# Performance work log

Hardware: AMD Instinct MI355X
Metric: run time of the kernel (lower is better)

## Reference

```python
import jax, jax.numpy as jnp
import numpy as np

N_NODES = 100000
N_EDGES = 1200000
N_GRAPHS = 1024
IN_DIM, HIDDEN, OUT_DIM = 4, 64, 2
BN_EPS = 1e-5


def setup_inputs() -> dict:
    key = jax.random.key(0)
    ks = jax.random.split(key, 12)
    x = jax.random.normal(ks[0], (N_NODES, IN_DIM), dtype=jnp.float32)
    edge_index = jax.random.randint(ks[1], (2, N_EDGES), 0, N_NODES, dtype=jnp.int64)
    batch = jnp.sort(jax.random.randint(ks[2], (N_NODES,), 0, N_GRAPHS, dtype=jnp.int64))
    s = 1.0 / np.sqrt(HIDDEN)
    return {
        "x": x,
        "edge_index": edge_index,
        "batch": batch,
        "W_enc": jax.random.normal(ks[3], (IN_DIM, HIDDEN), dtype=jnp.float32) * 0.5,
        "b_enc": jnp.zeros((HIDDEN,), dtype=jnp.float32),
        "bn_gamma": jnp.ones((HIDDEN,), dtype=jnp.float32),
        "bn_beta": jnp.zeros((HIDDEN,), dtype=jnp.float32),
        "bn_mean": jax.random.normal(ks[4], (HIDDEN,), dtype=jnp.float32) * 0.1,
        "bn_var": jax.random.uniform(ks[5], (HIDDEN,), dtype=jnp.float32, minval=0.5, maxval=1.5),
        "W_gcn": jax.random.normal(ks[6], (HIDDEN, HIDDEN), dtype=jnp.float32) * s,
        "b_gcn": jnp.zeros((HIDDEN,), dtype=jnp.float32),
        "W_cls1": jax.random.normal(ks[7], (HIDDEN, HIDDEN), dtype=jnp.float32) * s,
        "b_cls1": jnp.zeros((HIDDEN,), dtype=jnp.float32),
        "W_cls2": jax.random.normal(ks[8], (HIDDEN, OUT_DIM), dtype=jnp.float32) * s,
        "b_cls2": jnp.zeros((OUT_DIM,), dtype=jnp.float32),
    }


def reference(x, edge_index, batch, W_enc, b_enc, bn_gamma, bn_beta, bn_mean, bn_var,
              W_gcn, b_gcn, W_cls1, b_cls1, W_cls2, b_cls2):
    n = x.shape[0]
    # Encoder: Linear -> ReLU -> Dropout(eval=identity) -> BatchNorm1d (running stats)
    h = jnp.maximum(x @ W_enc + b_enc, 0.0)
    h = (h - bn_mean) * jax.lax.rsqrt(bn_var + BN_EPS) * bn_gamma + bn_beta
    # GCNConv (PyG): add self-loops, symmetric deg^{-1/2} normalization
    loop = jnp.arange(n, dtype=edge_index.dtype)
    src = jnp.concatenate([edge_index[0], loop])  # [E+N]
    dst = jnp.concatenate([edge_index[1], loop])
    deg = jnp.zeros((n,), dtype=h.dtype).at[dst].add(1.0)
    dis = jnp.where(deg > 0, jax.lax.rsqrt(jnp.maximum(deg, 1.0)), 0.0)
    norm = dis[src] * dis[dst]  # [E+N]
    hw = h @ W_gcn  # [N, H]
    msg = hw[src] * norm[:, None]  # gather + scale, [E+N, H]
    agg = jax.ops.segment_sum(msg, dst, num_segments=n) + b_gcn
    agg = jnp.maximum(agg, 0.0)  # .relu()
    # global_mean_pool over graphs
    sums = jax.ops.segment_sum(agg, batch, num_segments=N_GRAPHS)  # [G, H]
    cnts = jax.ops.segment_sum(jnp.ones((n,), dtype=agg.dtype), batch, num_segments=N_GRAPHS)
    gm = sums / jnp.maximum(cnts, 1.0)[:, None]
    # Classifier: Linear -> ReLU -> Dropout(eval) -> Linear
    out = jnp.maximum(gm @ W_cls1 + b_cls1, 0.0) @ W_cls2 + b_cls2
    return out
```

## Files before the change

### kernel.cpp

```cpp
#include <hip/hip_runtime.h>

#define N_NODES  100000
#define N_EDGES  1200000
#define N_GRAPHS 1024

#define BSH    9
#define BNODES 512
#define NBUCK  196
#define FBLK   512
#define CHUNK  ((N_EDGES + FBLK - 1) / FBLK)
#define ENC_BLOCKS 1563

__device__ __forceinline__ unsigned short f2bf(float f) {
  unsigned u = __float_as_uint(f);
  return (unsigned short)((u + 0x7fffu + ((u >> 16) & 1u)) >> 16);
}
__device__ __forceinline__ float bf2f(unsigned short b) {
  return __uint_as_float(((unsigned)b) << 16);
}

__global__ __launch_bounds__(256) void k_cnt(const int* __restrict__ ei,
                                             int* __restrict__ cnt,
                                             float* __restrict__ gsum) {
  __shared__ int h[NBUCK];
  int t = threadIdx.x;
  for (int i = t; i < NBUCK; i += 256) h[i] = 0;
  int gi = blockIdx.x * 256 + t;
  if (gi < N_GRAPHS * 64) gsum[gi] = 0.f;
  __syncthreads();
  int start = blockIdx.x * CHUNK, end = min(start + CHUNK, N_EDGES);
  for (int e = start + t; e < end; e += 256)
    atomicAdd(&h[ei[N_EDGES + e] >> BSH], 1);
  __syncthreads();
  for (int b = t; b < NBUCK; b += 256)
    cnt[b * FBLK + blockIdx.x] = h[b];
}

__global__ __launch_bounds__(256) void k_scan_enc(
    int* __restrict__ cnt, int* __restrict__ tot,
    const float* __restrict__ x,
    const float* __restrict__ Wenc, const float* __restrict__ benc,
    const float* __restrict__ gamma, const float* __restrict__ beta,
    const float* __restrict__ mean,  const float* __restrict__ var,
    const float* __restrict__ Wgcn,
    unsigned short* __restrict__ hw) {
  int t = threadIdx.x;
  int lane = t & 63, w = t >> 6;
  if (blockIdx.x < NBUCK) {
    __shared__ int wsum[4];
    int b = blockIdx.x;
    int v0 = cnt[b * FBLK + 2 * t], v1 = cnt[b * FBLK + 2 * t + 1];
    int a = v0 + v1;
    int incl = a;
    #pragma unroll
    for (int off = 1; off < 64; off <<= 1) {
      int y = __shfl_up(incl, off);
      if (lane >= off) incl += y;
    }
    if (lane == 63) wsum[w] = incl;
    __syncthreads();
    if (t == 0) {
      int s = 0;
      #pragma unroll
      for (int i = 0; i < 4; ++i) { int x2 = wsum[i]; wsum[i] = s; s += x2; }
      tot[b] = s;
    }
    __syncthreads();
    int excl = wsum[w] + incl - a;
    cnt[b * FBLK + 2 * t] = excl;
    cnt[b * FBLK + 2 * t + 1] = excl + v0;
    return;
  }
  int wv = (blockIdx.x - NBUCK) * 4 + w;
  if (wv >= 6250) return;
  float be = benc[lane];
  float sc = gamma[lane] * rsqrtf(var[lane] + 1e-5f);
  float mu = mean[lane], bt = beta[lane];
  float w0 = Wenc[lane], w1 = Wenc[64 + lane], w2 = Wenc[128 + lane], w3 = Wenc[192 + lane];
  float wreg[64];
  #pragma unroll
  for (int k = 0; k < 64; ++k) wreg[k] = Wgcn[k * 64 + lane];
  int n0 = wv * 16;
  for (int i = 0; i < 16; ++i) {
    int n = n0 + i;
    float4 xv = ((const float4*)x)[n];
    float h = fmaf(xv.w, w3, fmaf(xv.z, w2, fmaf(xv.y, w1, fmaf(xv.x, w0, be))));
    h = fmaxf(h, 0.f);
    float hbn = (h - mu) * sc + bt;
    int hb = __float_as_int(hbn);
    float a0 = 0.f, a1 = 0.f, a2 = 0.f, a3 = 0.f;
    #pragma unroll
    for (int k = 0; k < 64; k += 4) {
      a0 = fmaf(__int_as_float(__builtin_amdgcn_readlane(hb, k)),     wreg[k],     a0);
      a1 = fmaf(__int_as_float(__builtin_amdgcn_readlane(hb, k + 1)), wreg[k + 1], a1);
      a2 = fmaf(__int_as_float(__builtin_amdgcn_readlane(hb, k + 2)), wreg[k + 2], a2);
      a3 = fmaf(__int_as_float(__builtin_amdgcn_readlane(hb, k + 3)), wreg[k + 3], a3);
    }
    hw[(size_t)n * 64 + lane] = f2bf((a0 + a1) + (a2 + a3));
  }
}

__global__ __launch_bounds__(256) void k_fill(const int* __restrict__ ei,
                                              const int* __restrict__ cnt,
                                              const int* __restrict__ tot,
                                              int* __restrict__ binned) {
  __shared__ int cur[NBUCK];
  __shared__ int wsum[4];
  int t = threadIdx.x, blk = blockIdx.x;
  int lane = t & 63, w = t >> 6;
  int v = (t < NBUCK) ? tot[t] : 0;
  int incl = v;
  #pragma unroll
  for (int off = 1; off < 64; off <<= 1) {
    int y = __shfl_up(incl, off);
    if (lane >= off) incl += y;
  }
  if (lane == 63) wsum[w] = incl;
  __syncthreads();
  if (t == 0) {
    int s = 0;
    #pragma unroll
    for (int i = 0; i < 4; ++i) { int x2 = wsum[i]; wsum[i] = s; s += x2; }
  }
  __syncthreads();
  if (t < NBUCK) cur[t] = (wsum[w] + incl - v) + cnt[t * FBLK + blk];
  __syncthreads();
  int start = blk * CHUNK, end = min(start + CHUNK, N_EDGES);
  for (int e = start + t; e < end; e += 256) {
    int src = ei[e];
    int dst = ei[N_EDGES + e];
    int b = dst >> BSH;
    int p = atomicAdd(&cur[b], 1);
    binned[p] = src | ((dst & (BNODES - 1)) << 17);
  }
}

__global__ __launch_bounds__(512) void k_csr(const int* __restrict__ tot,
                                             const int* __restrict__ binned,
                                             int* __restrict__ csr,
                                             int* __restrict__ row_start,
                                             float* __restrict__ dis) {
  __shared__ int hist[BNODES];
  __shared__ int wsum[8];
  __shared__ int b0S;
  int t = threadIdx.x;
  int blk = blockIdx.x;
  int lane = t & 63, w = t >> 6;
  int pv = (t < blk) ? tot[t] : 0;
  #pragma unroll
  for (int off = 32; off > 0; off >>= 1) pv += __shfl_down(pv, off);
  if (lane == 0) wsum[w] = pv;
  hist[t] = 0;
  __syncthreads();
  if (t == 0) {
    int s = 0;
    #pragma unroll
    for (int i = 0; i < 8; ++i) s += wsum[i];
    b0S = s;
  }
  __syncthreads();
  int b0 = b0S;
  int nE = tot[blk];
  int node0 = blk << BSH;
  for (int i = t; i < nE; i += 512)
    atomicAdd(&hist[(unsigned)binned[b0 + i] >> 17], 1);
  __syncthreads();
  int v = hist[t];
  int incl = v;
  #pragma unroll
  for (int off = 1; off < 64; off <<= 1) {
    int y = __shfl_up(incl, off);
    if (lane >= off) incl += y;
  }
  if (lane == 63) wsum[w] = incl;
  __syncthreads();
  if (t == 0) {
    int s = 0;
    #pragma unroll
    for (int i = 0; i < 8; ++i) { int x2 = wsum[i]; wsum[i] = s; s += x2; }
  }
  __syncthreads();
  int excl = wsum[w] + incl - v;
  hist[t] = excl;
  int node = node0 + t;
  if (node < N_NODES) {
    row_start[node] = b0 + excl;
    dis[node] = rsqrtf((float)(v + 1));
  }
  if (t == 0 && blk == NBUCK - 1) row_start[N_NODES] = N_EDGES;
  __syncthreads();
  for (int i = t; i < nE; i += 512) {
    int vv = binned[b0 + i];
    int d = (unsigned)vv >> 17;
    int p = atomicAdd(&hist[d], 1);
    csr[b0 + p] = vv & 0x1FFFF;
  }
}

__global__ __launch_bounds__(64) void k_gather(
    const int* __restrict__ row_start, const int* __restrict__ csr,
    const float* __restrict__ dis, const unsigned short* __restrict__ hw,
    const int* __restrict__ batch, const float* __restrict__ bgcn,
    float* __restrict__ gsum) {
  int lane = threadIdx.x;
  int nb = blockIdx.x * 4;
  float bias = bgcn[lane];
  float vout[4];
  int gid[4];
  #pragma unroll
  for (int k = 0; k < 4; ++k) {
    int n = nb + k;
    int st = row_start[n], en = row_start[n + 1];
    float dn = rsqrtf((float)(en - st + 1));
    float a0 = 0.f, a1 = 0.f, a2 = 0.f, a3 = 0.f;
    for (int c = st; c < en; c += 64) {
      int m = min(64, en - c);
      int idx = c + lane;
      int chunk = 0; float dv = 0.f;
      if (idx < en) { chunk = csr[idx]; dv = dis[chunk]; }
      int dvb = __float_as_int(dv);
      int j = 0;
      for (; j + 4 <= m; j += 4) {
        int s0 = __builtin_amdgcn_readlane(chunk, j);
        int s1 = __builtin_amdgcn_readlane(chunk, j + 1);
        int s2 = __builtin_amdgcn_readlane(chunk, j + 2);
        int s3 = __builtin_amdgcn_readlane(chunk, j + 3);
        float d0 = __int_as_float(__builtin_amdgcn_readlane(dvb, j));
        float d1 = __int_as_float(__builtin_amdgcn_readlane(dvb, j + 1));
        float d2 = __int_as_float(__builtin_amdgcn_readlane(dvb, j + 2));
        float d3 = __int_as_float(__builtin_amdgcn_readlane(dvb, j + 3));
        a0 = fmaf(d0, bf2f(hw[(size_t)s0 * 64 + lane]), a0);
        a1 = fmaf(d1, bf2f(hw[(size_t)s1 * 64 + lane]), a1);
        a2 = fmaf(d2, bf2f(hw[(size_t)s2 * 64 + lane]), a2);
        a3 = fmaf(d3, bf2f(hw[(size_t)s3 * 64 + lane]), a3);
      }
      for (; j < m; ++j) {
        int s = __builtin_amdgcn_readlane(chunk, j);
        float d = __int_as_float(__builtin_amdgcn_readlane(dvb, j));
        a0 = fmaf(d, bf2f(hw[(size_t)s * 64 + lane]), a0);
      }
    }
    float self = bf2f(hw[(size_t)n * 64 + lane]);
    float sum = (a0 + a1) + (a2 + a3);
    vout[k] = fmaxf(dn * fmaf(dn, self, sum) + bias, 0.f);
    gid[k] = batch[n];
  }
  float vs = vout[0];
  int cg = gid[0];
  #pragma unroll
  for (int k = 1; k < 4; ++k) {
    if (gid[k] == cg) vs += vout[k];
    else {
      atomicAdd(&gsum[cg * 64 + lane], vs);
      vs = vout[k]; cg = gid[k];
    }
  }
  atomicAdd(&gsum[cg * 64 + lane], vs);
}

__global__ void k_cls(const float* __restrict__ gsum, const int* __restrict__ batch,
                      const float* __restrict__ W1, const float* __restrict__ b1,
                      const float* __restrict__ W2, const float* __restrict__ b2,
                      float* __restrict__ out) {
  __shared__ float gm[64];
  __shared__ int cntS;
  int j = threadIdx.x;
  int g = blockIdx.x;
  if (j == 0) {
    int lo = 0, hi = N_NODES;
    while (lo < hi) { int mid = (lo + hi) >> 1; if (batch[mid] < g) lo = mid + 1; else hi = mid; }
    int lo2 = lo, hi2 = N_NODES;
    while (lo2 < hi2) { int mid = (lo2 + hi2) >> 1; if (batch[mid] < g + 1) lo2 = mid + 1; else hi2 = mid; }
    cntS = lo2 - lo;
  }
  __syncthreads();
  float denom = fmaxf((float)cntS, 1.0f);
  gm[j] = gsum[g * 64 + j] / denom;
  __syncthreads();
  float hid = b1[j];
  #pragma unroll
  for (int k = 0; k < 64; ++k) hid += gm[k] * W1[k * 64 + j];
  hid = fmaxf(hid, 0.f);
  float o0 = hid * W2[j * 2 + 0];
  float o1 = hid * W2[j * 2 + 1];
  #pragma unroll
  for (int off = 32; off > 0; off >>= 1) {
    o0 += __shfl_down(o0, off);
    o1 += __shfl_down(o1, off);
  }
  if (j == 0) {
    out[g * 2 + 0] = o0 + b2[0];
    out[g * 2 + 1] = o1 + b2[1];
  }
}

extern "C" void kernel_launch(void* const* d_in, const int* in_sizes, int n_in,
                              void* d_out, int out_size, void* d_ws, size_t ws_size,
                              hipStream_t stream) {
  const float* x     = (const float*)d_in[0];
  const int*   ei    = (const int*)d_in[1];
  const int*   batch = (const int*)d_in[2];
  const float* Wenc  = (const float*)d_in[3];
  const float* benc  = (const float*)d_in[4];
  const float* gamma = (const float*)d_in[5];
  const float* beta  = (const float*)d_in[6];
  const float* mean  = (const float*)d_in[7];
  const float* var   = (const float*)d_in[8];
  const float* Wgcn  = (const float*)d_in[9];
  const float* bgcn  = (const float*)d_in[10];
  const float* W1    = (const float*)d_in[11];
  const float* b1    = (const float*)d_in[12];
  const float* W2    = (const float*)d_in[13];
  const float* b2    = (const float*)d_in[14];
  float* out = (float*)d_out;

  char* ws = (char*)d_ws;
  float*          gsum      = (float*)ws;          ws += (size_t)N_GRAPHS * 64 * 4;
  int*            cnt       = (int*)ws;            ws += (size_t)NBUCK * FBLK * 4;
  int*            tot       = (int*)ws;            ws += 256 * 4;
  int*            binned    = (int*)ws;            ws += (size_t)N_EDGES * 4;
  int*            csr       = (int*)ws;            ws += (size_t)N_EDGES * 4;
  int*            row_start = (int*)ws;            ws += (size_t)(N_NODES + 32) * 4;
  float*          dis       = (float*)ws;          ws += (size_t)N_NODES * 4;
  unsigned short* hw        = (unsigned short*)ws; ws += (size_t)N_NODES * 64 * 2;

  k_cnt<<<FBLK, 256, 0, stream>>>(ei, cnt, gsum);
  k_scan_enc<<<NBUCK + ENC_BLOCKS, 256, 0, stream>>>(cnt, tot, x, Wenc, benc,
                                                     gamma, beta, mean, var, Wgcn, hw);
  k_fill<<<FBLK, 256, 0, stream>>>(ei, cnt, tot, binned);
  k_csr<<<NBUCK, 512, 0, stream>>>(tot, binned, csr, row_start, dis);
  k_gather<<<(N_NODES / 4), 64, 0, stream>>>(row_start, csr, dis, hw, batch, bgcn, gsum);
  k_cls<<<N_GRAPHS, 64, 0, stream>>>(gsum, batch, W1, b1, W2, b2, out);
}
```

Measured before the change: 190.6 us.

## Halve CSR bucket size and co-schedule edge counting with encoder

Bucket width drops from 512 to 256 nodes, giving 391 buckets. k_csr now runs 391 blocks of 256 threads instead of 196 blocks of 512, which gives more parallelism in the CSR build. The edge-count histogram is merged into the encoder launch so counting and encoding run concurrently, and the scan becomes its own kernel. The fill kernel's bucket scan now handles two buckets per thread. The number of launches stays the same, and the cnt array and per-block bucket-offset work both grow.

```diff
diff --git a/kernel.cpp b/kernel.cpp
--- a/kernel.cpp
+++ b/kernel.cpp
@@ -4,9 +4,9 @@
 #define N_EDGES  1200000
 #define N_GRAPHS 1024
 
-#define BSH    9
-#define BNODES 512
-#define NBUCK  196
+#define BSH    8
+#define BNODES 256
+#define NBUCK  391
 #define FBLK   512
 #define CHUNK  ((N_EDGES + FBLK - 1) / FBLK)
 #define ENC_BLOCKS 1563
@@ -19,25 +19,8 @@
   return __uint_as_float(((unsigned)b) << 16);
 }
 
-__global__ __launch_bounds__(256) void k_cnt(const int* __restrict__ ei,
-                                             int* __restrict__ cnt,
-                                             float* __restrict__ gsum) {
-  __shared__ int h[NBUCK];
-  int t = threadIdx.x;
-  for (int i = t; i < NBUCK; i += 256) h[i] = 0;
-  int gi = blockIdx.x * 256 + t;
-  if (gi < N_GRAPHS * 64) gsum[gi] = 0.f;
-  __syncthreads();
-  int start = blockIdx.x * CHUNK, end = min(start + CHUNK, N_EDGES);
-  for (int e = start + t; e < end; e += 256)
-    atomicAdd(&h[ei[N_EDGES + e] >> BSH], 1);
-  __syncthreads();
-  for (int b = t; b < NBUCK; b += 256)
-    cnt[b * FBLK + blockIdx.x] = h[b];
-}
-
-__global__ __launch_bounds__(256) void k_scan_enc(
-    int* __restrict__ cnt, int* __restrict__ tot,
+__global__ __launch_bounds__(256) void k_cnt_enc(
+    const int* __restrict__ ei, int* __restrict__ cnt, float* __restrict__ gsum,
     const float* __restrict__ x,
     const float* __restrict__ Wenc, const float* __restrict__ benc,
     const float* __restrict__ gamma, const float* __restrict__ beta,
@@ -46,32 +29,21 @@
     unsigned short* __restrict__ hw) {
   int t = threadIdx.x;
   int lane = t & 63, w = t >> 6;
-  if (blockIdx.x < NBUCK) {
-    __shared__ int wsum[4];
-    int b = blockIdx.x;
-    int v0 = cnt[b * FBLK + 2 * t], v1 = cnt[b * FBLK + 2 * t + 1];
-    int a = v0 + v1;
-    int incl = a;
-    #pragma unroll
-    for (int off = 1; off < 64; off <<= 1) {
-      int y = __shfl_up(incl, off);
-      if (lane >= off) incl += y;
-    }
-    if (lane == 63) wsum[w] = incl;
+  if (blockIdx.x < FBLK) {
+    __shared__ int h[NBUCK];
+    for (int i = t; i < NBUCK; i += 256) h[i] = 0;
+    int gi = blockIdx.x * 256 + t;
+    if (gi < N_GRAPHS * 64) gsum[gi] = 0.f;
     __syncthreads();
-    if (t == 0) {
-      int s = 0;
-      #pragma unroll
-      for (int i = 0; i < 4; ++i) { int x2 = wsum[i]; wsum[i] = s; s += x2; }
-      tot[b] = s;
-    }
+    int start = blockIdx.x * CHUNK, end = min(start + CHUNK, N_EDGES);
+    for (int e = start + t; e < end; e += 256)
+      atomicAdd(&h[ei[N_EDGES + e] >> BSH], 1);
     __syncthreads();
-    int excl = wsum[w] + incl - a;
-    cnt[b * FBLK + 2 * t] = excl;
-    cnt[b * FBLK + 2 * t + 1] = excl + v0;
+    for (int b = t; b < NBUCK; b += 256)
+      cnt[b * FBLK + blockIdx.x] = h[b];
     return;
   }
-  int wv = (blockIdx.x - NBUCK) * 4 + w;
+  int wv = (blockIdx.x - FBLK) * 4 + w;
   if (wv >= 6250) return;
   float be = benc[lane];
   float sc = gamma[lane] * rsqrtf(var[lane] + 1e-5f);
@@ -100,6 +72,33 @@
   }
 }
 
+__global__ __launch_bounds__(256) void k_scan(int* __restrict__ cnt,
+                                              int* __restrict__ tot) {
+  __shared__ int wsum[4];
+  int b = blockIdx.x, t = threadIdx.x;
+  int lane = t & 63, w = t >> 6;
+  int v0 = cnt[b * FBLK + 2 * t], v1 = cnt[b * FBLK + 2 * t + 1];
+  int a = v0 + v1;
+  int incl = a;
+  #pragma unroll
+  for (int off = 1; off < 64; off <<= 1) {
+    int y = __shfl_up(incl, off);
+    if (lane >= off) incl += y;
+  }
+  if (lane == 63) wsum[w] = incl;
+  __syncthreads();
+  if (t == 0) {
+    int s = 0;
+    #pragma unroll
+    for (int i = 0; i < 4; ++i) { int x2 = wsum[i]; wsum[i] = s; s += x2; }
+    tot[b] = s;
+  }
+  __syncthreads();
+  int excl = wsum[w] + incl - a;
+  cnt[b * FBLK + 2 * t] = excl;
+  cnt[b * FBLK + 2 * t + 1] = excl + v0;
+}
+
 __global__ __launch_bounds__(256) void k_fill(const int* __restrict__ ei,
                                               const int* __restrict__ cnt,
                                               const int* __restrict__ tot,
@@ -108,8 +107,11 @@
   __shared__ int wsum[4];
   int t = threadIdx.x, blk = blockIdx.x;
   int lane = t & 63, w = t >> 6;
-  int v = (t < NBUCK) ? tot[t] : 0;
-  int incl = v;
+  int b0i = 2 * t, b1i = 2 * t + 1;
+  int v0 = (b0i < NBUCK) ? tot[b0i] : 0;
+  int v1 = (b1i < NBUCK) ? tot[b1i] : 0;
+  int a = v0 + v1;
+  int incl = a;
   #pragma unroll
   for (int off = 1; off < 64; off <<= 1) {
     int y = __shfl_up(incl, off);
@@ -123,7 +125,9 @@
     for (int i = 0; i < 4; ++i) { int x2 = wsum[i]; wsum[i] = s; s += x2; }
   }
   __syncthreads();
-  if (t < NBUCK) cur[t] = (wsum[w] + incl - v) + cnt[t * FBLK + blk];
+  int exclPair = wsum[w] + incl - a;
+  if (b0i < NBUCK) cur[b0i] = exclPair + cnt[b0i * FBLK + blk];
+  if (b1i < NBUCK) cur[b1i] = exclPair + v0 + cnt[b1i * FBLK + blk];
   __syncthreads();
   int start = blk * CHUNK, end = min(start + CHUNK, N_EDGES);
   for (int e = start + t; e < end; e += 256) {
@@ -135,18 +139,19 @@
   }
 }
 
-__global__ __launch_bounds__(512) void k_csr(const int* __restrict__ tot,
+__global__ __launch_bounds__(256) void k_csr(const int* __restrict__ tot,
                                              const int* __restrict__ binned,
                                              int* __restrict__ csr,
                                              int* __restrict__ row_start,
                                              float* __restrict__ dis) {
   __shared__ int hist[BNODES];
-  __shared__ int wsum[8];
+  __shared__ int wsum[4];
   __shared__ int b0S;
   int t = threadIdx.x;
   int blk = blockIdx.x;
   int lane = t & 63, w = t >> 6;
-  int pv = (t < blk) ? tot[t] : 0;
+  int pv = 0;
+  for (int i = t; i < blk; i += 256) pv += tot[i];
   #pragma unroll
   for (int off = 32; off > 0; off >>= 1) pv += __shfl_down(pv, off);
   if (lane == 0) wsum[w] = pv;
@@ -155,14 +160,14 @@
   if (t == 0) {
     int s = 0;
     #pragma unroll
-    for (int i = 0; i < 8; ++i) s += wsum[i];
+    for (int i = 0; i < 4; ++i) s += wsum[i];
     b0S = s;
   }
   __syncthreads();
   int b0 = b0S;
   int nE = tot[blk];
   int node0 = blk << BSH;
-  for (int i = t; i < nE; i += 512)
+  for (int i = t; i < nE; i += 256)
     atomicAdd(&hist[(unsigned)binned[b0 + i] >> 17], 1);
   __syncthreads();
   int v = hist[t];
@@ -177,7 +182,7 @@
   if (t == 0) {
     int s = 0;
     #pragma unroll
-    for (int i = 0; i < 8; ++i) { int x2 = wsum[i]; wsum[i] = s; s += x2; }
+    for (int i = 0; i < 4; ++i) { int x2 = wsum[i]; wsum[i] = s; s += x2; }
   }
   __syncthreads();
   int excl = wsum[w] + incl - v;
@@ -189,7 +194,7 @@
   }
   if (t == 0 && blk == NBUCK - 1) row_start[N_NODES] = N_EDGES;
   __syncthreads();
-  for (int i = t; i < nE; i += 512) {
+  for (int i = t; i < nE; i += 256) {
     int vv = binned[b0 + i];
     int d = (unsigned)vv >> 17;
     int p = atomicAdd(&hist[d], 1);
@@ -317,18 +322,18 @@
   char* ws = (char*)d_ws;
   float*          gsum      = (float*)ws;          ws += (size_t)N_GRAPHS * 64 * 4;
   int*            cnt       = (int*)ws;            ws += (size_t)NBUCK * FBLK * 4;
-  int*            tot       = (int*)ws;            ws += 256 * 4;
+  int*            tot       = (int*)ws;            ws += 512 * 4;
   int*            binned    = (int*)ws;            ws += (size_t)N_EDGES * 4;
   int*            csr       = (int*)ws;            ws += (size_t)N_EDGES * 4;
   int*            row_start = (int*)ws;            ws += (size_t)(N_NODES + 32) * 4;
   float*          dis       = (float*)ws;          ws += (size_t)N_NODES * 4;
   unsigned short* hw        = (unsigned short*)ws; ws += (size_t)N_NODES * 64 * 2;
 
-  k_cnt<<<FBLK, 256, 0, stream>>>(ei, cnt, gsum);
-  k_scan_enc<<<NBUCK + ENC_BLOCKS, 256, 0, stream>>>(cnt, tot, x, Wenc, benc,
-                                                     gamma, beta, mean, var, Wgcn, hw);
+  k_cnt_enc<<<FBLK + ENC_BLOCKS, 256, 0, stream>>>(ei, cnt, gsum, x, Wenc, benc,
+                                                   gamma, beta, mean, var, Wgcn, hw);
+  k_scan<<<NBUCK, 256, 0, stream>>>(cnt, tot);
   k_fill<<<FBLK, 256, 0, stream>>>(ei, cnt, tot, binned);
-  k_csr<<<NBUCK, 512, 0, stream>>>(tot, binned, csr, row_start, dis);
+  k_csr<<<NBUCK, 256, 0, stream>>>(tot, binned, csr, row_start, dis);
   k_gather<<<(N_NODES / 4), 64, 0, stream>>>(row_start, csr, dis, hw, batch, bgcn, gsum);
   k_cls<<<N_GRAPHS, 64, 0, stream>>>(gsum, batch, W1, b1, W2, b2, out);
 }
```

Measured after the change: 190.8 us. No clear change (+0.1%).
